# Performance work log

Hardware: AMD Instinct MI355X
Metric: run time of the kernel (lower is better)

## Reference

```python
import jax, jax.numpy as jnp
import numpy as np

HID = 64      # hidden_dim
HEADS = 4     # attention heads
CH = HID // HEADS  # 16 per-head channels
EDIM = 6      # edge_dim
NEG = 0.2     # leaky_relu negative slope


def _glorot(key, shape):
    fan_in, fan_out = shape[0], shape[-1]
    s = np.sqrt(6.0 / (fan_in + fan_out)).astype(np.float32)
    return jax.random.uniform(key, shape, jnp.float32, -s, s)


def setup_inputs() -> dict:
    key = jax.random.key(0)
    ks = iter(jax.random.split(key, 48))
    N, E, T = 100000, 1200000, 20000
    inp = {
        "x": jax.random.normal(next(ks), (N, 7), jnp.float32),
        "pos": jax.random.normal(next(ks), (N, 3), jnp.float32),
        "node_type": jax.random.randint(next(ks), (N,), 0, 2),
        "edge_index": jax.random.randint(next(ks), (2, E), 0, N),
        "edge_attr": jax.random.normal(next(ks), (E, EDIM), jnp.float32),
        "num_tracks": T,
        "hidden_state": jax.random.normal(next(ks), (T, HID), jnp.float32),
        # params
        "type_emb": jax.random.normal(next(ks), (2, 8), jnp.float32),
        "enc_W1": _glorot(next(ks), (18, HID)), "enc_b1": jnp.zeros((HID,), jnp.float32),
        "enc_W2": _glorot(next(ks), (HID, HID)), "enc_b2": jnp.zeros((HID,), jnp.float32),
        "gru_Wi": _glorot(next(ks), (HID, 3 * HID)), "gru_bi": jnp.zeros((3 * HID,), jnp.float32),
        "gru_Wh": _glorot(next(ks), (HID, 3 * HID)), "gru_bh": jnp.zeros((3 * HID,), jnp.float32),
        "dec_W1": _glorot(next(ks), (HID, HID)), "dec_b1": jnp.zeros((HID,), jnp.float32),
        "dec_W2": _glorot(next(ks), (HID, 7)), "dec_b2": jnp.zeros((7,), jnp.float32),
    }
    for g in ("g1", "g2"):
        inp[g + "_Wl"] = _glorot(next(ks), (HID, HID))
        inp[g + "_bl"] = jnp.zeros((HID,), jnp.float32)
        inp[g + "_Wr"] = _glorot(next(ks), (HID, HID))
        inp[g + "_br"] = jnp.zeros((HID,), jnp.float32)
        inp[g + "_We"] = _glorot(next(ks), (EDIM, HID))
        inp[g + "_att"] = _glorot(next(ks), (HEADS, CH))
        inp[g + "_bias"] = jnp.zeros((HID,), jnp.float32)
    return inp


def _segment_softmax(e, seg, n):
    m = jax.ops.segment_max(e, seg, num_segments=n)
    m = jnp.where(jnp.isfinite(m), m, 0.0)
    ex = jnp.exp(e - m[seg])
    s = jax.ops.segment_sum(ex, seg, num_segments=n)
    return ex / (s[seg] + 1e-16)


def _gatv2(h, src, dst, eattr, Wl, bl, Wr, br, We, att, bias):
    N = h.shape[0]
    xl = (h @ Wl + bl).reshape(N, HEADS, CH)
    xr = (h @ Wr + br).reshape(N, HEADS, CH)
    ea = (eattr @ We).reshape(-1, HEADS, CH)
    g = jax.nn.leaky_relu(xl[src] + xr[dst] + ea, NEG)      # [E, H, C]
    e = jnp.einsum('ehc,hc->eh', g, att)                     # [E, H]
    alpha = _segment_softmax(e, dst, N)                      # [E, H]
    msg = xl[src] * alpha[..., None]                         # [E, H, C]
    out = jax.ops.segment_sum(msg, dst, num_segments=N)
    return out.reshape(N, HID) + bias, alpha


def reference(x, pos, node_type, edge_index, edge_attr, num_tracks, hidden_state,
              type_emb, enc_W1, enc_b1, enc_W2, enc_b2,
              g1_Wl, g1_bl, g1_Wr, g1_br, g1_We, g1_att, g1_bias,
              g2_Wl, g2_bl, g2_Wr, g2_br, g2_We, g2_att, g2_bias,
              gru_Wi, gru_bi, gru_Wh, gru_bh,
              dec_W1, dec_b1, dec_W2, dec_b2):
    N = x.shape[0]
    h = jnp.concatenate([x, pos, type_emb[node_type]], axis=-1)
    h = jax.nn.relu(h @ enc_W1 + enc_b1) @ enc_W2 + enc_b2

    # PyG GATv2Conv: add self loops, edge_attr fill_value='mean' (mean of incoming edges)
    src, dst = edge_index[0], edge_index[1]
    deg = jax.ops.segment_sum(jnp.ones(src.shape[0], jnp.float32), dst, num_segments=N)
    loop_attr = jax.ops.segment_sum(edge_attr, dst, num_segments=N) / jnp.maximum(deg, 1.0)[:, None]
    ar = jnp.arange(N)
    src_a = jnp.concatenate([src, ar])
    dst_a = jnp.concatenate([dst, ar])
    eattr_a = jnp.concatenate([edge_attr, loop_attr], axis=0)

    h1, a1 = _gatv2(h, src_a, dst_a, eattr_a, g1_Wl, g1_bl, g1_Wr, g1_br, g1_We, g1_att, g1_bias)
    h1 = jax.nn.relu(h1)
    h2, a2 = _gatv2(h1, src_a, dst_a, eattr_a, g2_Wl, g2_bl, g2_Wr, g2_br, g2_We, g2_att, g2_bias)

    # GRUCell on the first num_tracks nodes
    ht = h2[:num_tracks]
    gi = ht @ gru_Wi + gru_bi
    gh = hidden_state @ gru_Wh + gru_bh
    r = jax.nn.sigmoid(gi[:, :HID] + gh[:, :HID])
    z = jax.nn.sigmoid(gi[:, HID:2 * HID] + gh[:, HID:2 * HID])
    n = jnp.tanh(gi[:, 2 * HID:] + r * gh[:, 2 * HID:])
    new_tracks = (1.0 - z) * n + z * hidden_state

    new_full = jnp.concatenate([new_tracks, h2[num_tracks:]], axis=0)
    out = jax.nn.relu(new_full @ dec_W1 + dec_b1) @ dec_W2 + dec_b2  # [N, 7]
    final = out.at[:, :3].set(pos + out[:, :3])
    final = final.at[:, 3:6].set(x[:, :3] + out[:, 3:6])
    return final, new_full, a1, a2
```

## Files before the change

kernel.cpp:

```cpp
#include <hip/hip_runtime.h>

#define NEG 0.2f
#define LOG2E 1.44269504088896f
typedef unsigned short u16;

__device__ __forceinline__ float sigmoidf_(float v){ return 1.f/(1.f+__expf(-v)); }
__device__ __forceinline__ int rfl_(int v){ return __builtin_amdgcn_readfirstlane(v); }
__device__ __forceinline__ float bf2f_(unsigned u){ return __uint_as_float(u<<16); }
__device__ __forceinline__ u16 f2bf_(float f){
  unsigned u = __float_as_uint(f);
  u += 0x7FFFu + ((u>>16)&1u);
  return (u16)(u>>16);
}
template<int C>
__device__ __forceinline__ float dppadd_(float p){
  int r = __builtin_amdgcn_update_dpp(0, __float_as_int(p), C, 0xF, 0xF, true);
  return p + __int_as_float(r);
}
__device__ __forceinline__ float dppsum16_(float p){
  p = dppadd_<0x121>(p);
  p = dppadd_<0x122>(p);
  p = dppadd_<0x124>(p);
  p = dppadd_<0x128>(p);
  return p;
}

__global__ __launch_bounds__(256) void encdeg_kernel(
    const float* __restrict__ x, const float* __restrict__ pos,
    const int* __restrict__ ntype, const float* __restrict__ temb,
    const float* __restrict__ W1, const float* __restrict__ b1,
    const float* __restrict__ W2, const float* __restrict__ b2,
    float* __restrict__ hout,
    const int* __restrict__ ei, int* __restrict__ deg,
    int encB, int E, int N)
{
  __shared__ float sW1[18*64];
  __shared__ float sW2[4096];
  __shared__ float fT[4][8*20];
  __shared__ float tT[4][8*64];
  if ((int)blockIdx.x >= encB){
    int e = ((int)blockIdx.x - encB)*256 + threadIdx.x;
    if (e < E) atomicAdd(deg + ei[E+e], 1);
    return;
  }
  for (int i=threadIdx.x; i<18*64; i+=256) sW1[i]=W1[i];
  for (int i=threadIdx.x; i<4096; i+=256)  sW2[i]=W2[i];
  __syncthreads();
  int lane = threadIdx.x & 63;
  int wid  = threadIdx.x >> 6;
  int n0 = (blockIdx.x*4 + wid)*8;
  if (n0 >= N) return;
  float b1v=b1[lane], b2v=b2[lane];
  #pragma unroll
  for (int m=0;m<8;m++){
    int n=n0+m; float fv=0.f;
    if (n<N){
      if (lane<7)       fv=x[(size_t)n*7+lane];
      else if (lane<10) fv=pos[(size_t)n*3+lane-7];
      else if (lane<18) fv=temb[ntype[n]*8+lane-10];
    }
    if (lane<20) fT[wid][m*20+lane]=fv;
  }
  float t[8];
  #pragma unroll
  for (int m=0;m<8;m++) t[m]=b1v;
  #pragma unroll 2
  for (int k=0;k<18;k++){
    float w=sW1[k*64+lane];
    #pragma unroll
    for (int m=0;m<8;m++) t[m] += fT[wid][m*20+k]*w;
  }
  #pragma unroll
  for (int m=0;m<8;m++){ t[m]=fmaxf(t[m],0.f); tT[wid][m*64+lane]=t[m]; }
  float o[8];
  #pragma unroll
  for (int m=0;m<8;m++) o[m]=b2v;
  #pragma unroll 2
  for (int k=0;k<64;k++){
    float w=sW2[k*64+lane];
    #pragma unroll
    for (int m=0;m<8;m++) o[m] += tT[wid][m*64+k]*w;
  }
  #pragma unroll
  for (int m=0;m<8;m++){ int n=n0+m; if (n<N) hout[(size_t)n*64+lane]=o[m]; }
}

__global__ __launch_bounds__(256) void alloc_kernel(
    const int* __restrict__ deg, int* __restrict__ offs, int* __restrict__ counter, int N)
{
  __shared__ int wsum[4], woff[4], sbase;
  int lane = threadIdx.x & 63, w = threadIdx.x >> 6;
  int base = blockIdx.x*1024 + threadIdx.x*4;
  int v[4]; int s=0;
  #pragma unroll
  for (int j=0;j<4;j++){ int i=base+j; v[j]=(i<N)?deg[i]:0; s+=v[j]; }
  int inc=s;
  #pragma unroll
  for (int d=1;d<64;d<<=1){ int t=__shfl_up(inc,d); if (lane>=d) inc+=t; }
  if (lane==63) wsum[w]=inc;
  __syncthreads();
  if (threadIdx.x==0){
    woff[0]=0; woff[1]=wsum[0]; woff[2]=wsum[0]+wsum[1]; woff[3]=wsum[0]+wsum[1]+wsum[2];
    sbase = atomicAdd(counter, woff[3]+wsum[3]);
  }
  __syncthreads();
  int excl = sbase + woff[w] + (inc - s);
  #pragma unroll
  for (int j=0;j<4;j++){ int i=base+j; if (i<N) offs[i]=excl; excl+=v[j]; }
}

__global__ __launch_bounds__(256) void xfrmfill_kernel(
    const float* __restrict__ hin,
    const float* __restrict__ Wl, const float* __restrict__ bl,
    const float* __restrict__ Wr, const float* __restrict__ br,
    u16* __restrict__ xlo, u16* __restrict__ xro,
    const int* __restrict__ ei, const int* __restrict__ offs,
    int* __restrict__ cursor, int2* __restrict__ csr2,
    int xfB, int E, int N)
{
  __shared__ float hT[4][16*64];
  if ((int)blockIdx.x >= xfB){
    int e = ((int)blockIdx.x - xfB)*256 + threadIdx.x;
    if (e < E){
      int dst = ei[E + e];
      int p = atomicAdd(cursor + dst, 1);
      csr2[offs[dst] + p] = make_int2(e, ei[e]);
    }
    return;
  }
  int lane=threadIdx.x&63;
  int wid=threadIdx.x>>6;
  int n0=(blockIdx.x*4+wid)*16;
  if (n0>=N) return;
  #pragma unroll
  for (int m=0;m<16;m++){
    int n=n0+m;
    hT[wid][m*64+lane] = (n<N)? hin[(size_t)n*64+lane] : 0.f;
  }
  float blv=bl[lane], brv=br[lane];
  float al[16], ar[16];
  #pragma unroll
  for (int m=0;m<16;m++){ al[m]=blv; ar[m]=brv; }
  #pragma unroll 2
  for (int k=0;k<64;k++){
    float wl=Wl[k*64+lane], wr=Wr[k*64+lane];
    #pragma unroll
    for (int m=0;m<16;m++){
      float hb = hT[wid][m*64+k];
      al[m]+=hb*wl; ar[m]+=hb*wr;
    }
  }
  #pragma unroll
  for (int m=0;m<16;m++){
    int n=n0+m;
    if (n<N){ xlo[(((unsigned)n)<<6)+lane]=f2bf_(al[m]); xro[(((unsigned)n)<<6)+lane]=f2bf_(ar[m]); }
  }
}

__global__ __launch_bounds__(256) void xfrm_kernel(
    const float* __restrict__ hin,
    const float* __restrict__ Wl, const float* __restrict__ bl,
    const float* __restrict__ Wr, const float* __restrict__ br,
    u16* __restrict__ xlo, u16* __restrict__ xro, int N)
{
  __shared__ float sWl[4096], sWr[4096];
  __shared__ float hT[4][16*64];
  for (int i=threadIdx.x;i<4096;i+=256){ sWl[i]=Wl[i]; sWr[i]=Wr[i]; }
  __syncthreads();
  int lane=threadIdx.x&63;
  int wid=threadIdx.x>>6;
  int n0=(blockIdx.x*4+wid)*16;
  if (n0>=N) return;
  #pragma unroll
  for (int m=0;m<16;m++){
    int n=n0+m;
    hT[wid][m*64+lane] = (n<N)? hin[(size_t)n*64+lane] : 0.f;
  }
  float blv=bl[lane], brv=br[lane];
  float al[16], ar[16];
  #pragma unroll
  for (int m=0;m<16;m++){ al[m]=blv; ar[m]=brv; }
  #pragma unroll 2
  for (int k=0;k<64;k++){
    float wl=sWl[k*64+lane], wr=sWr[k*64+lane];
    #pragma unroll
    for (int m=0;m<16;m++){
      float hb = hT[wid][m*64+k];
      al[m]+=hb*wl; ar[m]+=hb*wr;
    }
  }
  #pragma unroll
  for (int m=0;m<16;m++){
    int n=n0+m;
    if (n<N){ xlo[(((unsigned)n)<<6)+lane]=f2bf_(al[m]); xro[(((unsigned)n)<<6)+lane]=f2bf_(ar[m]); }
  }
}

#define EDGE_STEP(EIDX, EADD, XV) do {                                       \
    float s_ = (XV) + xrv + (EADD);                                          \
    s_ = fmaxf(s_, NEG*s_);                                                  \
    float p_ = dppsum16_(s_*attv);                                           \
    if (isbase) aout[(((unsigned)(EIDX))<<2)+h] = p_;                        \
    if (__all(p_ <= mmax)) {                                                 \
      float w_ = exp2f(p_ - mmax);                                           \
      ssum += w_; acc += w_*(XV);                                            \
    } else {                                                                 \
      float mn_ = fmaxf(mmax, p_);                                           \
      float sc_ = exp2f(mmax - mn_);                                         \
      float w_  = exp2f(p_ - mn_);                                           \
      ssum = ssum*sc_ + w_;                                                  \
      acc  = acc*sc_ + w_*(XV);                                              \
      mmax = mn_;                                                            \
    }                                                                        \
  } while(0)

#define EDGE_PRE(J) \
    int e##J = rfl_(c##J.x), s##J = rfl_(c##J.y); \
    const float2* q##J = (const float2*)(eattr + (unsigned)e##J*6u); \
    float2 A##J=q##J[0], B##J=q##J[1], C##J=q##J[2]; \
    unsigned xv##J = xlb[(((unsigned)s##J)<<6)+lane];

#define EDGE_BODY(J) \
    float d##J = A##J.x*we0 + A##J.y*we1 + B##J.x*we2 + B##J.y*we3 + C##J.x*we4 + C##J.y*we5; \
    dsum += d##J; \
    EDGE_STEP(e##J, d##J, bf2f_(xv##J));

__global__ __launch_bounds__(256) void gat_kernel(
    const int2* __restrict__ csr2, const int* __restrict__ offs, const int* __restrict__ deg,
    const float* __restrict__ eattr,
    const u16* __restrict__ xlb, const u16* __restrict__ xrb,
    const float* __restrict__ We, const float* __restrict__ att,
    const float* __restrict__ bias,
    float* __restrict__ aout, float2* __restrict__ msbuf,
    float* __restrict__ hout,
    int E, int N, int do_relu)
{
  int lane = threadIdx.x & 63;
  int n = blockIdx.x*4 + (threadIdx.x>>6);
  if (n >= N) return;
  float we0=We[lane], we1=We[64+lane], we2=We[128+lane],
        we3=We[192+lane], we4=We[256+lane], we5=We[320+lane];
  float attv = att[lane] * LOG2E;
  float bv = bias[lane];
  float xrv = bf2f_(xrb[(((unsigned)n)<<6)+lane]);
  int h = lane >> 4;
  bool isbase = (lane & 15) == 0;
  int o0 = rfl_(offs[n]);
  int dg = rfl_(deg[n]);
  int oend = o0 + dg;
  float mmax = -3.402823e38f, ssum=0.f, acc=0.f, dsum=0.f;
  int o = o0;
  for (; o+4 <= oend; o += 4){
    int2 c0=csr2[o], c1=csr2[o+1], c2=csr2[o+2], c3=csr2[o+3];
    EDGE_PRE(0); EDGE_PRE(1); EDGE_PRE(2); EDGE_PRE(3);
    EDGE_BODY(0); EDGE_BODY(1); EDGE_BODY(2); EDGE_BODY(3);
  }
  for (; o < oend; ++o){
    int2 c0=csr2[o];
    EDGE_PRE(0);
    EDGE_BODY(0);
  }
  {
    float dS = dsum * (1.f/fmaxf((float)dg,1.f));
    float xvS = bf2f_((unsigned)xlb[(((unsigned)n)<<6)+lane]);
    EDGE_STEP(E+n, dS, xvS);
  }
  float sinv = 1.f/(ssum + 1e-16f);
  if (isbase) msbuf[(((unsigned)n)<<2)+h] = make_float2(mmax, sinv);
  float outv = acc*sinv + bv;
  if (do_relu) outv = fmaxf(outv, 0.f);
  hout[(((unsigned)n)<<6)+lane] = outv;
}

__global__ __launch_bounds__(256) void grudecalpha_kernel(
    const float* __restrict__ h2, const float* __restrict__ hid,
    const float* __restrict__ Wi, const float* __restrict__ bi,
    const float* __restrict__ Wh, const float* __restrict__ bh,
    const int* __restrict__ Tptr,
    const float* __restrict__ W1, const float* __restrict__ b1,
    const float* __restrict__ W2, const float* __restrict__ b2,
    const float* __restrict__ x, const float* __restrict__ pos,
    float* __restrict__ nf, float* __restrict__ fout,
    const int* __restrict__ ei,
    const float2* __restrict__ ms1, const float2* __restrict__ ms2,
    float4* __restrict__ a1, float4* __restrict__ a2,
    int gdB, int E, int N)
{
  __shared__ float sW1[4096];
  __shared__ float sW2[448];
  __shared__ float sb2[8];
  __shared__ float tT[4][8*68];
  __shared__ float pT[4][8*68];
  if ((int)blockIdx.x >= gdB){
    int e = ((int)blockIdx.x - gdB)*256 + threadIdx.x;
    if (e < E+N){
      int dst = (e<E)? ei[E+e] : (e-E);
      {
        float4 r = a1[e];
        const float2* mp = ms1 + (((unsigned)dst)<<2);
        float2 m0=mp[0], m1=mp[1], m2=mp[2], m3=mp[3];
        float4 o;
        o.x = exp2f(r.x - m0.x)*m0.y;
        o.y = exp2f(r.y - m1.x)*m1.y;
        o.z = exp2f(r.z - m2.x)*m2.y;
        o.w = exp2f(r.w - m3.x)*m3.y;
        a1[e] = o;
      }
      {
        float4 r = a2[e];
        const float2* mp = ms2 + (((unsigned)dst)<<2);
        float2 m0=mp[0], m1=mp[1], m2=mp[2], m3=mp[3];
        float4 o;
        o.x = exp2f(r.x - m0.x)*m0.y;
        o.y = exp2f(r.y - m1.x)*m1.y;
        o.z = exp2f(r.z - m2.x)*m2.y;
        o.w = exp2f(r.w - m3.x)*m3.y;
        a2[e] = o;
      }
    }
    return;
  }
  for (int i=threadIdx.x;i<4096;i+=256) sW1[i]=W1[i];
  for (int i=threadIdx.x;i<448;i+=256) sW2[i]=W2[i];
  if (threadIdx.x<7)  sb2[threadIdx.x]=b2[threadIdx.x];
  __syncthreads();
  int lane = threadIdx.x & 63;
  int wid  = threadIdx.x >> 6;
  int n0 = (blockIdx.x*4 + wid)*8;
  if (n0 >= N) return;
  int T = *Tptr;
  float hv[8], nfv[8];
  #pragma unroll
  for (int m=0;m<8;m++){ int n=n0+m; hv[m] = (n<N)? h2[(size_t)n*64+lane] : 0.f; }
  if (n0 < T){
    float pv[8];
    #pragma unroll
    for (int m=0;m<8;m++){ int n=n0+m; pv[m] = (n<T)? hid[(size_t)n*64+lane] : 0.f; }
    #pragma unroll
    for (int m=0;m<8;m++){ tT[wid][m*68+lane]=hv[m]; pT[wid][m*68+lane]=pv[m]; }
    float gr[8],gz[8],gn[8],hr[8],hz[8],hn[8];
    #pragma unroll
    for (int m=0;m<8;m++){ gr[m]=0.f;gz[m]=0.f;gn[m]=0.f;hr[m]=0.f;hz[m]=0.f;hn[m]=0.f; }
    for (int k=0;k<64;k++){
      float wir=Wi[k*192+lane], wiz=Wi[k*192+64+lane], win=Wi[k*192+128+lane];
      float whr=Wh[k*192+lane], whz=Wh[k*192+64+lane], whn=Wh[k*192+128+lane];
      #pragma unroll
      for (int m=0;m<8;m++){
        float a=tT[wid][m*68+k], b=pT[wid][m*68+k];
        gr[m]+=a*wir; gz[m]+=a*wiz; gn[m]+=a*win;
        hr[m]+=b*whr; hz[m]+=b*whz; hn[m]+=b*whn;
      }
    }
    float bir=bi[lane], biz=bi[64+lane], bin=bi[128+lane];
    float bhr=bh[lane], bhz=bh[64+lane], bhn=bh[128+lane];
    #pragma unroll
    for (int m=0;m<8;m++){
      int n=n0+m;
      if (n<T){
        float r  = sigmoidf_(gr[m]+bir + hr[m]+bhr);
        float z  = sigmoidf_(gz[m]+biz + hz[m]+bhz);
        float nn = tanhf(gn[m]+bin + r*(hn[m]+bhn));
        nfv[m] = (1.f-z)*nn + z*pv[m];
      } else {
        nfv[m] = hv[m];
      }
    }
  } else {
    #pragma unroll
    for (int m=0;m<8;m++) nfv[m] = hv[m];
  }
  #pragma unroll
  for (int m=0;m<8;m++){ int n=n0+m; if (n<N) nf[(size_t)n*64+lane]=nfv[m]; }
  #pragma unroll
  for (int m=0;m<8;m++) tT[wid][m*68+lane]=nfv[m];
  float t[8];
  float b1v=b1[lane];
  #pragma unroll
  for (int m=0;m<8;m++) t[m]=b1v;
  #pragma unroll 2
  for (int k=0;k<64;k++){
    float w=sW1[k*64+lane];
    #pragma unroll
    for (int m=0;m<8;m++) t[m] += tT[wid][m*68+k]*w;
  }
  #pragma unroll
  for (int m=0;m<8;m++) t[m]=fmaxf(t[m],0.f);
  #pragma unroll
  for (int m=0;m<8;m++) tT[wid][m*68+lane]=t[m];
  int mm = lane >> 3, cc = lane & 7;
  if (cc < 7){
    float a2v = sb2[cc];
    #pragma unroll 4
    for (int k=0;k<64;k++) a2v += tT[wid][mm*68+k]*sW2[k*7+cc];
    int n = n0+mm;
    if (n < N){
      if (cc<3)      a2v += pos[(size_t)n*3+cc];
      else if (cc<6) a2v += x[(size_t)n*7+(cc-3)];
      fout[(size_t)n*7+cc] = a2v;
    }
  }
}

extern "C" void kernel_launch(void* const* d_in, const int* in_sizes, int n_in,
                              void* d_out, int out_size, void* d_ws, size_t ws_size,
                              hipStream_t stream)
{
  const float* x     = (const float*)d_in[0];
  const float* pos   = (const float*)d_in[1];
  const int*   ntype = (const int*)d_in[2];
  const int*   eidx  = (const int*)d_in[3];
  const float* eattr = (const float*)d_in[4];
  const int*   Tptr  = (const int*)d_in[5];
  const float* hid   = (const float*)d_in[6];
  const float* temb  = (const float*)d_in[7];
  const float* encW1 = (const float*)d_in[8];
  const float* encb1 = (const float*)d_in[9];
  const float* encW2 = (const float*)d_in[10];
  const float* encb2 = (const float*)d_in[11];
  const float* gruWi = (const float*)d_in[12];
  const float* grubi = (const float*)d_in[13];
  const float* gruWh = (const float*)d_in[14];
  const float* grubh = (const float*)d_in[15];
  const float* decW1 = (const float*)d_in[16];
  const float* decb1 = (const float*)d_in[17];
  const float* decW2 = (const float*)d_in[18];
  const float* decb2 = (const float*)d_in[19];
  const float* gWl[2]  = {(const float*)d_in[20], (const float*)d_in[27]};
  const float* gbl[2]  = {(const float*)d_in[21], (const float*)d_in[28]};
  const float* gWr[2]  = {(const float*)d_in[22], (const float*)d_in[29]};
  const float* gbr[2]  = {(const float*)d_in[23], (const float*)d_in[30]};
  const float* gWe[2]  = {(const float*)d_in[24], (const float*)d_in[31]};
  const float* gatt[2] = {(const float*)d_in[25], (const float*)d_in[32]};
  const float* gbias[2]= {(const float*)d_in[26], (const float*)d_in[33]};

  int N  = in_sizes[0] / 7;
  int E  = in_sizes[3] / 2;
  int Ea = E + N;

  char* w = (char*)d_ws;
  float* A      = (float*)w; w += (size_t)N*64*sizeof(float);
  float* B      = (float*)w; w += (size_t)N*64*sizeof(float);
  u16*   XL     = (u16*)w;  w += (size_t)N*64*sizeof(u16);
  u16*   XR     = (u16*)w;  w += (size_t)N*64*sizeof(u16);
  int*   deg    = (int*)w;   w += (size_t)N*sizeof(int);
  int*   cursor = (int*)w;   w += (size_t)N*sizeof(int);
  int*   counter= (int*)w;   w += 4*sizeof(int);
  int*   offs   = (int*)w;   w += (size_t)N*sizeof(int);
  float2* msbuf1= (float2*)w; w += (size_t)N*4*sizeof(float2);
  float2* msbuf2= (float2*)w; w += (size_t)N*4*sizeof(float2);
  int2*  csr2   = (int2*)w;  w += (size_t)E*sizeof(int2);

  float* out_final = (float*)d_out;
  float* out_nf    = out_final + (size_t)N*7;
  float* out_a1    = out_nf + (size_t)N*64;
  float* out_a2    = out_a1 + (size_t)Ea*4;

  hipMemsetAsync(deg, 0, ((size_t)2*N + 4)*sizeof(int), stream);

  int encB = (N+31)/32;
  int degB = (E+255)/256;
  encdeg_kernel<<<encB+degB, 256, 0, stream>>>(x,pos,ntype,temb,encW1,encb1,encW2,encb2,A,
      eidx, deg, encB, E, N);

  alloc_kernel<<<(N+1023)/1024, 256, 0, stream>>>(deg, offs, counter, N);

  int xfB = (N+63)/64;
  int flB = (E+255)/256;
  xfrmfill_kernel<<<xfB+flB, 256, 0, stream>>>(A, gWl[0], gbl[0], gWr[0], gbr[0], XL, XR,
      eidx, offs, cursor, csr2, xfB, E, N);

  gat_kernel<<<(N+3)/4, 256, 0, stream>>>(csr2, offs, deg, eattr, XL, XR,
      gWe[0], gatt[0], gbias[0], out_a1, msbuf1, B, E, N, 1);

  xfrm_kernel<<<xfB, 256, 0, stream>>>(B, gWl[1], gbl[1], gWr[1], gbr[1], XL, XR, N);
  gat_kernel<<<(N+3)/4, 256, 0, stream>>>(csr2, offs, deg, eattr, XL, XR,
      gWe[1], gatt[1], gbias[1], out_a2, msbuf2, A, E, N, 0);

  int gdB = (N+31)/32;
  int alB = (Ea+255)/256;
  grudecalpha_kernel<<<gdB+alB, 256, 0, stream>>>(A, hid, gruWi, grubi, gruWh, grubh, Tptr,
      decW1, decb1, decW2, decb2, x, pos, out_nf, out_final,
      eidx, msbuf1, msbuf2, (float4*)out_a1, (float4*)out_a2, gdB, E, N);
}
```

Measured before the change: 553.9 us.

## Pack edge attributes into CSR slots to avoid random gathers in GAT

During the CSR fill, each edge's id, source and its six edge-attribute floats are written into a 32-byte slot in destination order. Both GAT passes then read that contiguous slot instead of gathering edge_attr at random edge indices. This removes two dependent random gathers per edge per layer. In exchange the fill kernel scatters four times more bytes, and the workspace is reordered so the first GAT layer writes into buffer A instead of a separate buffer B.

After: 509.1 us. -8.1%, faster.

```diff
diff --git a/kernel.cpp b/kernel.cpp
--- a/kernel.cpp
+++ b/kernel.cpp
@@ -114,8 +114,9 @@
     const float* __restrict__ Wl, const float* __restrict__ bl,
     const float* __restrict__ Wr, const float* __restrict__ br,
     u16* __restrict__ xlo, u16* __restrict__ xro,
-    const int* __restrict__ ei, const int* __restrict__ offs,
-    int* __restrict__ cursor, int2* __restrict__ csr2,
+    const int* __restrict__ ei, const float* __restrict__ eattr,
+    const int* __restrict__ offs,
+    int* __restrict__ cursor, float4* __restrict__ slots,
     int xfB, int E, int N)
 {
   __shared__ float hT[4][16*64];
@@ -124,7 +125,15 @@
     if (e < E){
       int dst = ei[E + e];
       int p = atomicAdd(cursor + dst, 1);
-      csr2[offs[dst] + p] = make_int2(e, ei[e]);
+      const float2* ep = (const float2*)(eattr + (size_t)e*6);
+      float2 p0=ep[0], p1=ep[1], p2=ep[2];
+      float4 a, b;
+      a.x = __int_as_float(e); a.y = __int_as_float(ei[e]);
+      a.z = p0.x; a.w = p0.y;
+      b.x = p1.x; b.y = p1.y; b.z = p2.x; b.w = p2.y;
+      unsigned slot = (unsigned)(offs[dst] + p);
+      slots[slot*2u]   = a;
+      slots[slot*2u+1] = b;
     }
     return;
   }
@@ -214,20 +223,19 @@
     }                                                                        \
   } while(0)
 
-#define EDGE_PRE(J) \
-    int e##J = rfl_(c##J.x), s##J = rfl_(c##J.y); \
-    const float2* q##J = (const float2*)(eattr + (unsigned)e##J*6u); \
-    float2 A##J=q##J[0], B##J=q##J[1], C##J=q##J[2]; \
+#define EDGE_PRE(J, OO) \
+    float4 u##J = slots[(unsigned)(OO)*2u], v##J = slots[(unsigned)(OO)*2u+1u]; \
+    int e##J = rfl_(__float_as_int(u##J.x)); \
+    int s##J = rfl_(__float_as_int(u##J.y)); \
     unsigned xv##J = xlb[(((unsigned)s##J)<<6)+lane];
 
 #define EDGE_BODY(J) \
-    float d##J = A##J.x*we0 + A##J.y*we1 + B##J.x*we2 + B##J.y*we3 + C##J.x*we4 + C##J.y*we5; \
+    float d##J = u##J.z*we0 + u##J.w*we1 + v##J.x*we2 + v##J.y*we3 + v##J.z*we4 + v##J.w*we5; \
     dsum += d##J; \
     EDGE_STEP(e##J, d##J, bf2f_(xv##J));
 
 __global__ __launch_bounds__(256) void gat_kernel(
-    const int2* __restrict__ csr2, const int* __restrict__ offs, const int* __restrict__ deg,
-    const float* __restrict__ eattr,
+    const float4* __restrict__ slots, const int* __restrict__ offs, const int* __restrict__ deg,
     const u16* __restrict__ xlb, const u16* __restrict__ xrb,
     const float* __restrict__ We, const float* __restrict__ att,
     const float* __restrict__ bias,
@@ -251,13 +259,11 @@
   float mmax = -3.402823e38f, ssum=0.f, acc=0.f, dsum=0.f;
   int o = o0;
   for (; o+4 <= oend; o += 4){
-    int2 c0=csr2[o], c1=csr2[o+1], c2=csr2[o+2], c3=csr2[o+3];
-    EDGE_PRE(0); EDGE_PRE(1); EDGE_PRE(2); EDGE_PRE(3);
+    EDGE_PRE(0,o); EDGE_PRE(1,o+1); EDGE_PRE(2,o+2); EDGE_PRE(3,o+3);
     EDGE_BODY(0); EDGE_BODY(1); EDGE_BODY(2); EDGE_BODY(3);
   }
   for (; o < oend; ++o){
-    int2 c0=csr2[o];
-    EDGE_PRE(0);
+    EDGE_PRE(0,o);
     EDGE_BODY(0);
   }
   {
@@ -439,16 +445,15 @@
 
   char* w = (char*)d_ws;
   float* A      = (float*)w; w += (size_t)N*64*sizeof(float);
-  float* B      = (float*)w; w += (size_t)N*64*sizeof(float);
   u16*   XL     = (u16*)w;  w += (size_t)N*64*sizeof(u16);
   u16*   XR     = (u16*)w;  w += (size_t)N*64*sizeof(u16);
+  float2* msbuf1= (float2*)w; w += (size_t)N*4*sizeof(float2);
+  float2* msbuf2= (float2*)w; w += (size_t)N*4*sizeof(float2);
+  float4* slots = (float4*)w; w += (size_t)E*32;
   int*   deg    = (int*)w;   w += (size_t)N*sizeof(int);
   int*   cursor = (int*)w;   w += (size_t)N*sizeof(int);
   int*   counter= (int*)w;   w += 4*sizeof(int);
   int*   offs   = (int*)w;   w += (size_t)N*sizeof(int);
-  float2* msbuf1= (float2*)w; w += (size_t)N*4*sizeof(float2);
-  float2* msbuf2= (float2*)w; w += (size_t)N*4*sizeof(float2);
-  int2*  csr2   = (int2*)w;  w += (size_t)E*sizeof(int2);
 
   float* out_final = (float*)d_out;
   float* out_nf    = out_final + (size_t)N*7;
@@ -467,13 +472,13 @@
   int xfB = (N+63)/64;
   int flB = (E+255)/256;
   xfrmfill_kernel<<<xfB+flB, 256, 0, stream>>>(A, gWl[0], gbl[0], gWr[0], gbr[0], XL, XR,
-      eidx, offs, cursor, csr2, xfB, E, N);
-
-  gat_kernel<<<(N+3)/4, 256, 0, stream>>>(csr2, offs, deg, eattr, XL, XR,
-      gWe[0], gatt[0], gbias[0], out_a1, msbuf1, B, E, N, 1);
-
-  xfrm_kernel<<<xfB, 256, 0, stream>>>(B, gWl[1], gbl[1], gWr[1], gbr[1], XL, XR, N);
-  gat_kernel<<<(N+3)/4, 256, 0, stream>>>(csr2, offs, deg, eattr, XL, XR,
+      eidx, eattr, offs, cursor, slots, xfB, E, N);
+
+  gat_kernel<<<(N+3)/4, 256, 0, stream>>>(slots, offs, deg, XL, XR,
+      gWe[0], gatt[0], gbias[0], out_a1, msbuf1, A, E, N, 1);
+
+  xfrm_kernel<<<xfB, 256, 0, stream>>>(A, gWl[1], gbl[1], gWr[1], gbr[1], XL, XR, N);
+  gat_kernel<<<(N+3)/4, 256, 0, stream>>>(slots, offs, deg, XL, XR,
       gWe[1], gatt[1], gbias[1], out_a2, msbuf2, A, E, N, 0);
 
   int gdB = (N+31)/32;
```
